# Performance work log

Hardware: AMD Instinct MI355X
Metric: run time of the kernel (lower is better)

## Reference

```python
import jax, jax.numpy as jnp
import numpy as np

H = 512       # hidden_dim == node_init_dim
N_MAX = 128   # max nodes (upper bound on ADD_NODE count)
L = 1024      # action sequence length (padded with -1)
NEG = -1e9    # mask value for invalid destination logits


def _gru(x, h, wih, whh, bih, bhh):
    # PyTorch nn.GRUCell math; gates packed as [r, z, n] along dim 0.
    gi = wih @ x + bih
    gh = whh @ h + bhh
    d = h.shape[0]
    r = jax.nn.sigmoid(gi[:d] + gh[:d])
    z = jax.nn.sigmoid(gi[d:2 * d] + gh[d:2 * d])
    n = jnp.tanh(gi[2 * d:] + r * gh[2 * d:])
    return (1.0 - z) * n + z * h


def _make_actions(rng):
    # Synthesize a grammatically valid DGMG teacher-forcing trace:
    # ADD_NODE=0, ADD_EDGE=1, CHOOSE_DEST=2, STOP_EDGE=3, STOP_NODE=4, pad=-1
    acts, ags = [], []
    cur = -1
    while len(acts) < L - 8 and cur < N_MAX - 1:
        acts.append(0); ags.append(0)
        cur += 1
        if cur > 0:
            for _ in range(int(rng.integers(1, 4))):
                if len(acts) >= L - 4:
                    break
                acts.append(1); ags.append(0)
                acts.append(2); ags.append(int(rng.integers(0, cur)))
            acts.append(3); ags.append(0)
    acts.append(4); ags.append(0)
    pad = L - len(acts)
    acts += [-1] * pad
    ags += [0] * pad
    return np.array(acts, np.int64), np.array(ags, np.int64)


def setup_inputs() -> dict:
    rng = np.random.default_rng(0)
    acts, ags = _make_actions(rng)
    key = jax.random.key(0)
    ks = jax.random.split(key, 12)
    s = 0.02
    p = lambda k, shape: jax.random.normal(k, shape, jnp.float32) * s
    return {
        "actions": jnp.asarray(acts),
        "args_seq": jnp.asarray(ags),
        "node_init": p(ks[0], (H,)),
        "w_nip": p(ks[1], (H, H)), "b_nip": jnp.zeros((H,), jnp.float32),
        "w_e1": p(ks[2], (H, 2 * H)), "b_e1": jnp.zeros((H,), jnp.float32),
        "w_e2": p(ks[3], (2, H)), "b_e2": jnp.zeros((2,), jnp.float32),
        "w_q": p(ks[4], (H, 2 * H)), "b_q": jnp.zeros((H,), jnp.float32),
        "w_k": p(ks[5], (H, H)), "b_k": jnp.zeros((H,), jnp.float32),
        "wih_n": p(ks[6], (3 * H, H)), "whh_n": p(ks[7], (3 * H, H)),
        "bih_n": jnp.zeros((3 * H,), jnp.float32), "bhh_n": jnp.zeros((3 * H,), jnp.float32),
        "wih_g": p(ks[8], (3 * H, H)), "whh_g": p(ks[9], (3 * H, H)),
        "bih_g": jnp.zeros((3 * H,), jnp.float32), "bhh_g": jnp.zeros((3 * H,), jnp.float32),
        "graph0": jnp.zeros((H,), jnp.float32),
    }


def reference(actions, args_seq, node_init, w_nip, b_nip, w_e1, b_e1, w_e2, b_e2,
              w_q, b_q, w_k, b_k, wih_n, whh_n, bih_n, bhh_n,
              wih_g, whh_g, bih_g, bhh_g, graph0):
    h0 = w_nip @ node_init + b_nip  # same fresh-node embedding for every ADD_NODE
    idx_range = jnp.arange(N_MAX)

    def edge_logits(g, curv):
        h = jax.nn.relu(w_e1 @ jnp.concatenate([g, curv]) + b_e1)
        return w_e2 @ h + b_e2  # (2,)

    def add_node(carry, arg):
        g, ne, cur, nll = carry
        cur2 = cur + 1
        ne2 = ne.at[cur2].set(h0)
        g2 = _gru(h0, g, wih_g, whh_g, bih_g, bhh_g)
        return (g2, ne2, cur2, nll)

    def add_edge(carry, arg):
        g, ne, cur, nll = carry
        nll2 = nll - jax.nn.log_softmax(edge_logits(g, ne[cur]))[0]
        return (g, ne, cur, nll2)

    def choose_dest(carry, arg):
        g, ne, cur, nll = carry
        curv = ne[cur]
        q = w_q @ jnp.concatenate([g, curv]) + b_q           # (H,)
        k = ne @ w_k.T + b_k                                  # (N_MAX, H)
        logits = jnp.where(idx_range < cur, k @ q, NEG)       # mask nodes >= cur
        nll2 = nll - jax.nn.log_softmax(logits)[arg]
        chosen = ne[arg]
        new_cur = _gru(chosen, curv, wih_n, whh_n, bih_n, bhh_n)
        ne2 = ne.at[cur].set(new_cur)
        g2 = _gru(new_cur, g, wih_g, whh_g, bih_g, bhh_g)
        return (g2, ne2, cur, nll2)

    def stop_edge(carry, arg):
        g, ne, cur, nll = carry
        nll2 = nll - jax.nn.log_softmax(edge_logits(g, ne[cur]))[1]
        return (g, ne, cur, nll2)

    def noop(carry, arg):
        return carry

    branches = [add_node, add_edge, choose_dest, stop_edge, noop]

    def step(carry, inp):
        a, arg = inp
        idx = jnp.where((a < 0) | (a >= 4), 4, a).astype(jnp.int32)
        return jax.lax.switch(idx, branches, carry, arg), None

    init = (graph0, jnp.zeros((N_MAX, H), graph0.dtype),
            jnp.int32(-1), jnp.zeros((), graph0.dtype))
    (g, ne, cur, nll), _ = jax.lax.scan(
        step, init, (actions.astype(jnp.int32), args_seq.astype(jnp.int32)))
    return nll
```

## Files before the change

kernel.cpp:

```cpp
#include <hip/hip_runtime.h>
#include <math.h>

#define NBLK 64
#define NTHR 704
#define LSEQ 1024

typedef unsigned int u32;
typedef unsigned short u16;
typedef unsigned long long u64;

__device__ __forceinline__ float bf2f(u16 u){ union{u32 i;float f;}v; v.i=(u32)u<<16; return v.f; }
__device__ __forceinline__ u16 f2bf(float f){ union{float f;u32 i;}v; v.f=f; u32 x=v.i;
  return (u16)((x + 0x7fffu + ((x>>16)&1u)) >> 16); }
__device__ __forceinline__ float u2f(u32 u){ union{u32 i;float f;}v; v.i=u; return v.f; }
__device__ __forceinline__ u32  f2u(float f){ union{float f;u32 i;}v; v.f=f; return v.i; }
__device__ __forceinline__ float sigm(float x){ return 1.f/(1.f+__expf(-x)); }

__device__ __forceinline__ u64 gld64(const u64* p){ return __hip_atomic_load(const_cast<u64*>(p), __ATOMIC_RELAXED, __HIP_MEMORY_SCOPE_AGENT); }
__device__ __forceinline__ void gst64(u64* p, u64 v){ __hip_atomic_store(p, v, __ATOMIC_RELAXED, __HIP_MEMORY_SCOPE_AGENT); }
__device__ __forceinline__ u64 pollt(const u64* p, u32 tag){
  u64 v; int n = 0;
  do { v = gld64(p); } while ((u32)(v>>32) != tag && ++n < (1<<20));
  return v;
}

__device__ __forceinline__ float wred(float a){
  a += __int_as_float(__builtin_amdgcn_update_dpp(0, __float_as_int(a), 0x111, 0xf, 0xf, true));
  a += __int_as_float(__builtin_amdgcn_update_dpp(0, __float_as_int(a), 0x112, 0xf, 0xf, true));
  a += __int_as_float(__builtin_amdgcn_update_dpp(0, __float_as_int(a), 0x114, 0xf, 0xf, true));
  a += __int_as_float(__builtin_amdgcn_update_dpp(0, __float_as_int(a), 0x118, 0xf, 0xf, true));
  a += __int_as_float(__builtin_amdgcn_update_dpp(0, __float_as_int(a), 0x142, 0xa, 0xf, true));
  a += __int_as_float(__builtin_amdgcn_update_dpp(0, __float_as_int(a), 0x143, 0xc, 0xf, true));
  return __int_as_float(__builtin_amdgcn_readlane(__float_as_int(a), 63));
}
__device__ __forceinline__ float wredsh(float a){
  #pragma unroll
  for (int off = 32; off; off >>= 1) a += __shfl_xor(a, off);
  return a;
}
__device__ __forceinline__ float wredmaxsh(float a){
  #pragma unroll
  for (int off = 32; off; off >>= 1) a = fmaxf(a, __shfl_xor(a, off));
  return a;
}

__device__ __forceinline__ float dot8p(uint4 w, float4 a, float4 b2){
  float s;
  s  = u2f(w.x<<16)*a.x  + u2f(w.x&0xffff0000u)*a.y;
  s += u2f(w.y<<16)*a.z  + u2f(w.y&0xffff0000u)*a.w;
  s += u2f(w.z<<16)*b2.x + u2f(w.z&0xffff0000u)*b2.y;
  s += u2f(w.w<<16)*b2.z + u2f(w.w&0xffff0000u)*b2.w;
  return s;
}
__device__ __forceinline__ float dot4f(float4 w, float4 x){
  return w.x*x.x + w.y*x.y + w.z*x.z + w.w*x.w;
}
__device__ __forceinline__ uint4 pk8(float4 a, float4 b2){
  uint4 r;
  r.x = (u32)f2bf(a.x)  | ((u32)f2bf(a.y)<<16);
  r.y = (u32)f2bf(a.z)  | ((u32)f2bf(a.w)<<16);
  r.z = (u32)f2bf(b2.x) | ((u32)f2bf(b2.y)<<16);
  r.w = (u32)f2bf(b2.z) | ((u32)f2bf(b2.w)<<16);
  return r;
}

#define SMEM_BYTES 150048

#define RUN_JOBS() do { \
  if (wv == 8 && d2V && (b == d2o1 || b == d2o2)){ \
    int half_ = (b == d2o2) ? 1 : 0; \
    const u64* P_ = XP + ((size_t)(d2Slot*64 + lane))*64 + half_*32; \
    u64 vv_[32]; int bad_; int nn_ = 0; \
    do { bad_ = 0; \
      _Pragma("unroll") for (int j_ = 0; j_ < 32; ++j_) vv_[j_] = gld64(P_ + j_); \
      _Pragma("unroll") for (int j_ = 0; j_ < 32; ++j_) bad_ |= ((u32)(vv_[j_]>>32) != d2Tag); \
    } while (bad_ && ++nn_ < (1<<20)); \
    float h0_ = 0.f, h1_ = 0.f; \
    _Pragma("unroll") for (int j_ = 0; j_ < 32; ++j_){ \
      h0_ += bf2f((u16)(vv_[j_] & 0xffff)); h1_ += bf2f((u16)((vv_[j_]>>16) & 0xffff)); } \
    gst64(&XS[half_*256 + d2Slot*64 + lane], ((u64)d2Tag<<32) | (u32)f2bf(h0_) | ((u32)f2bf(h1_)<<16)); \
  } \
  if (wv == 10 && d3V && b == d3o1){ \
    const u64* pa_ = &XS[d3Slot*64 + lane]; \
    const u64* pb_ = &XS[256 + d3Slot*64 + lane]; \
    u64 va_, vb_; int nn_ = 0; \
    do { va_ = gld64(pa_); vb_ = gld64(pb_); } \
    while ((((u32)(va_>>32) != d3Tag) || ((u32)(vb_>>32) != d3Tag)) && ++nn_ < (1<<20)); \
    float x0 = bf2f((u16)(va_ & 0xffff)) + bf2f((u16)(vb_ & 0xffff)); \
    float x1 = bf2f((u16)((va_>>16) & 0xffff)) + bf2f((u16)((vb_>>16) & 0xffff)); \
    x0 = (lane < d3cur)      ? x0 : -__builtin_inff(); \
    x1 = (lane + 64 < d3cur) ? x1 : -__builtin_inff(); \
    float m_ = wredmaxsh(fmaxf(x0, x1)); \
    float s_ = wredsh(__expf(x0 - m_) + __expf(x1 - m_)); \
    float la_ = (d3arg < 64) ? __shfl(x0, d3arg) : __shfl(x1, d3arg - 64); \
    if (lane == 0) nllw += (m_ + logf(s_)) - la_; \
  } \
  if (wv == 9 && e2V && b == e2Own){ \
    u64 v_ = pollt(XE + e2Slot*64 + lane, e2Tag); \
    float p0_ = wredsh(bf2f((u16)(v_ & 0xffff))); \
    float p1_ = wredsh(bf2f((u16)((v_>>16) & 0xffff))); \
    if (lane == 0){ \
      float l0_ = p0_ + be2_0, l1_ = p1_ + be2_1; \
      float m_ = fmaxf(l0_, l1_); \
      nllw += m_ + logf(__expf(l0_-m_) + __expf(l1_-m_)) - (e2Sel ? l1_ : l0_); \
    } \
  } \
} while(0)

#define SHIFT3() do { \
  d3V=d2V; d3Slot=d2Slot; d3o1=d2o1; d3Tag=d2Tag; d3cur=d2cur; d3arg=d2arg; \
  d2V=d1V; d2Slot=d1Slot; d2o1=d1o1; d2o2=d1o2; d2Tag=d1Tag; d2cur=d1cur; d2arg=d1arg; \
  d1V=0; \
  e2V=e1V; e2Slot=e1Slot; e2Own=e1Own; e2Tag=e1Tag; e2Sel=e1Sel; \
  e1V=0; \
} while(0)

__global__ void __launch_bounds__(NTHR, 1)
dgmg_kernel(const int* __restrict__ actions, const int* __restrict__ argseq,
            const float* __restrict__ node_init, const float* __restrict__ w_nip, const float* __restrict__ b_nip,
            const float* __restrict__ w_e1, const float* __restrict__ b_e1,
            const float* __restrict__ w_e2, const float* __restrict__ b_e2,
            const float* __restrict__ w_q, const float* __restrict__ b_q,
            const float* __restrict__ w_k,
            const float* __restrict__ wih_n, const float* __restrict__ whh_n,
            const float* __restrict__ bih_n, const float* __restrict__ bhh_n,
            const float* __restrict__ wih_g, const float* __restrict__ whh_g,
            const float* __restrict__ bih_g, const float* __restrict__ bhh_g,
            const float* __restrict__ graph0,
            float* __restrict__ out, unsigned char* __restrict__ ws)
{
  extern __shared__ unsigned char smem[];
  u16* s_wihg = (u16*)smem;
  u16* s_whhg = s_wihg + 24*512;
  u16* s_wihn = s_whhg + 24*512;
  u16* s_whhn = s_wihn + 24*512;
  u16* s_we1  = s_whhn + 24*512;
  u16* s_wq   = s_we1 + 8*1024;
  float* s_g    = (float*)(s_wq + 8*1024);
  float* s_nc   = s_g + 512;
  float* s_curv = s_nc + 512;
  float* s_h0   = s_curv + 512;
  float* s_kloc = s_h0 + 512;
  float* s_bihg = s_kloc + 1024;
  float* s_bhhg = s_bihg + 24;
  float* s_bihn = s_bhhg + 24;
  float* s_bhhn = s_bihn + 24;
  float* s_be1  = s_bhhn + 24;
  float* s_bq   = s_be1 + 8;
  float* s_q8   = s_bq + 8;
  float* s_red  = s_q8 + 8;
  u16*   s_gin  = (u16*)(s_red + 16);

  const int b = blockIdx.x, tid = threadIdx.x;
  const int wv = tid >> 6, lane = tid & 63;
  const int d = b*8 + ((wv < 8) ? wv : 0);

  u64* Xng = (u64*)ws;
  u64* Xh  = Xng + 2048;
  u64* XE  = Xh + 512;
  u64* XP  = XE + 256;
  u64* XS  = XP + 16384;
  u64* XN  = XS + 512;

  if (tid < 24){
    int ld = tid/3, gt = tid%3;
    int row = gt*512 + b*8 + ld;
    s_bihg[tid] = bih_g[row]; s_bhhg[tid] = bhh_g[row];
    s_bihn[tid] = bih_n[row]; s_bhhn[tid] = bhh_n[row];
  }
  if (tid < 8){ s_be1[tid] = b_e1[b*8+tid]; s_bq[tid] = b_q[b*8+tid]; }

  for (int r = wv; r < 24; r += 11){
    int ld = r/3, gt = r%3;
    long grow = (long)(gt*512 + b*8 + ld) * 512;
    float4 a0, a1;
    a0 = *(const float4*)&wih_g[grow + lane*8]; a1 = *(const float4*)&wih_g[grow + lane*8 + 4];
    *(uint4*)&s_wihg[r*512 + lane*8] = pk8(a0, a1);
    a0 = *(const float4*)&whh_g[grow + lane*8]; a1 = *(const float4*)&whh_g[grow + lane*8 + 4];
    *(uint4*)&s_whhg[r*512 + lane*8] = pk8(a0, a1);
    a0 = *(const float4*)&wih_n[grow + lane*8]; a1 = *(const float4*)&wih_n[grow + lane*8 + 4];
    *(uint4*)&s_wihn[r*512 + lane*8] = pk8(a0, a1);
    a0 = *(const float4*)&whh_n[grow + lane*8]; a1 = *(const float4*)&whh_n[grow + lane*8 + 4];
    *(uint4*)&s_whhn[r*512 + lane*8] = pk8(a0, a1);
  }
  if (wv < 8){
    long grow = (long)(b*8 + wv) * 1024;
    #pragma unroll
    for (int h = 0; h < 2; ++h){
      float4 a0 = *(const float4*)&w_e1[grow + h*512 + lane*8];
      float4 a1 = *(const float4*)&w_e1[grow + h*512 + lane*8 + 4];
      *(uint4*)&s_we1[wv*1024 + h*512 + lane*8] = pk8(a0, a1);
      float4 q0 = *(const float4*)&w_q[grow + h*512 + lane*8];
      float4 q1 = *(const float4*)&w_q[grow + h*512 + lane*8 + 4];
      *(uint4*)&s_wq[wv*1024 + h*512 + lane*8] = pk8(q0, q1);
    }
  }
  float we2_0 = w_e2[d], we2_1 = w_e2[512+d];
  float be2_0 = b_e2[0], be2_1 = b_e2[1];
  float nllw = 0.f;

  int d1V=0,d1Slot=0,d1o1=0,d1o2=0,d1cur=0,d1arg=0; u32 d1Tag=0;
  int d2V=0,d2Slot=0,d2o1=0,d2o2=0,d2cur=0,d2arg=0; u32 d2Tag=0;
  int d3V=0,d3Slot=0,d3o1=0,d3cur=0,d3arg=0; u32 d3Tag=0;
  int e1V=0,e1Slot=0,e1Own=0,e1Sel=0; u32 e1Tag=0;
  int e2V=0,e2Slot=0,e2Own=0,e2Sel=0; u32 e2Tag=0;
  int ecnt=0, dcnt=0;

  if (tid < 512) s_g[tid] = node_init[tid];
  __syncthreads();
  float cbg_r=0,cbg_z=0,bg_ni=0,bg_nh=0, bh_gr=0,bh_gz=0;
  float bn_r=0,bn_z=0,bn_nh=0, fb_r=0,fb_z=0,fb_n=0, be1w=0,bqw=0;
  if (wv < 8){
    cbg_r = s_bihg[wv*3+0]+s_bhhg[wv*3+0];
    cbg_z = s_bihg[wv*3+1]+s_bhhg[wv*3+1];
    bg_ni = s_bihg[wv*3+2]; bg_nh = s_bhhg[wv*3+2];
    bh_gr = s_bhhg[wv*3+0]; bh_gz = s_bhhg[wv*3+1];
    bn_r = s_bhhn[wv*3+0]; bn_z = s_bhhn[wv*3+1]; bn_nh = s_bhhn[wv*3+2];
    fb_r = s_bihn[wv*3+0]; fb_z = s_bihn[wv*3+1]; fb_n = s_bihn[wv*3+2];
    be1w = s_be1[wv]; bqw = s_bq[wv];
    const float* wr = w_nip + (long)d*512;
    float4 wa = *(const float4*)&wr[lane*8], wb2 = *(const float4*)&wr[lane*8+4];
    float4 xa = *(float4*)&s_g[lane*8], xb = *(float4*)&s_g[lane*8+4];
    float h0d = wred(dot4f(wa,xa)+dot4f(wb2,xb)) + b_nip[d];
    if (lane == 0) gst64(&Xh[d], (1ull<<32) | f2u(h0d));
  }
  __syncthreads();
  u32 ph = 2;

  float gi0r=0,gi0z=0,gi0n=0, ghn0r=0,ghn0z=0,ghn0n=0;
  int cur = -1, have_se = 0;
  bool first_an = true;

  for (int t = 0; t < LSEQ; ++t){
    int a = actions[t];
    if (a == 1) continue;
    if (a == 3){ have_se = 1; continue; }
    if (a < 0 || a >= 4) continue;

    int t1 = (t+1 < LSEQ) ? actions[t+1] : -1;
    int nxt = (t1 == 1);
    int i2 = (t+2 < LSEQ) ? t+2 : LSEQ-1;
    int chn = nxt ? argseq[i2] : 0;

    u32 tg = ph-1;

    if (a == 0){
      int eslot = ecnt & 3;
      if (first_an){
        if (tid < 512){ u64 v = pollt(&Xh[tid], 1u); s_h0[tid] = u2f((u32)v); s_g[tid] = graph0[tid]; }
      } else {
        if (tid < 512){ u64 v = pollt(&Xng[((tg&1)*512+tid)*2+1], tg); s_g[tid] = u2f((u32)v); }
      }
      __syncthreads();
      RUN_JOBS();
      if (wv < 8){
        float4 xg_a = *(float4*)&s_g[lane*8], xg_b = *(float4*)&s_g[lane*8+4];
        float4 xc_a = *(float4*)&s_curv[lane*8], xc_b = *(float4*)&s_curv[lane*8+4];
        const u32* Whg = (const u32*)s_whhg;
        if (first_an){
          float4 xh_a = *(float4*)&s_h0[lane*8], xh_b = *(float4*)&s_h0[lane*8+4];
          const u32* Wig = (const u32*)s_wihg; const u32* Wn = (const u32*)s_whhn;
          gi0r = wred(dot8p(*(const uint4*)&Wig[(wv*3+0)*256+lane*4], xh_a,xh_b)) + s_bihg[wv*3+0];
          gi0z = wred(dot8p(*(const uint4*)&Wig[(wv*3+1)*256+lane*4], xh_a,xh_b)) + s_bihg[wv*3+1];
          gi0n = wred(dot8p(*(const uint4*)&Wig[(wv*3+2)*256+lane*4], xh_a,xh_b)) + s_bihg[wv*3+2];
          ghn0r = wred(dot8p(*(const uint4*)&Wn[(wv*3+0)*256+lane*4], xh_a,xh_b)) + bn_r;
          ghn0z = wred(dot8p(*(const uint4*)&Wn[(wv*3+1)*256+lane*4], xh_a,xh_b)) + bn_z;
          ghn0n = wred(dot8p(*(const uint4*)&Wn[(wv*3+2)*256+lane*4], xh_a,xh_b)) + bn_nh;
        }
        {
          float ghr = wred(dot8p(*(const uint4*)&Whg[(wv*3+0)*256+lane*4], xg_a,xg_b)) + bh_gr;
          float ghz = wred(dot8p(*(const uint4*)&Whg[(wv*3+1)*256+lane*4], xg_a,xg_b)) + bh_gz;
          float ghn = wred(dot8p(*(const uint4*)&Whg[(wv*3+2)*256+lane*4], xg_a,xg_b)) + bg_nh;
          float r_ = sigm(gi0r + ghr), z_ = sigm(gi0z + ghz);
          float n_ = tanhf(gi0n + r_*ghn);
          if (lane == 0) gst64(&Xng[((ph&1)*512+d)*2+1], ((u64)ph<<32) | f2u((1.f-z_)*n_ + z_*s_g[d]));
        }
        float fr=0.f, fz=0.f, fn=0.f;
        if (cur >= 0){
          const u32* Win = (const u32*)s_wihn;
          fr = wred(dot8p(*(const uint4*)&Win[(wv*3+0)*256+lane*4], xc_a,xc_b)) + fb_r;
          fz = wred(dot8p(*(const uint4*)&Win[(wv*3+1)*256+lane*4], xc_a,xc_b)) + fb_z;
          fn = wred(dot8p(*(const uint4*)&Win[(wv*3+2)*256+lane*4], xc_a,xc_b)) + fb_n;
          const float* wkr = w_k + (long)d*512;
          float4 ka = *(const float4*)&wkr[lane*8], kb2 = *(const float4*)&wkr[lane*8+4];
          float kv = wred(dot4f(ka,xc_a)+dot4f(kb2,xc_b));
          if (lane == 0){
            s_gin[cur*24+wv*3+0] = f2bf(fr); s_gin[cur*24+wv*3+1] = f2bf(fz); s_gin[cur*24+wv*3+2] = f2bf(fn);
            s_kloc[wv*128 + cur] = kv;
          }
        }
        if (nxt){
          float gr = (chn == cur) ? fr : bf2f(s_gin[chn*24+wv*3+0]);
          float gz = (chn == cur) ? fz : bf2f(s_gin[chn*24+wv*3+1]);
          float gn = (chn == cur) ? fn : bf2f(s_gin[chn*24+wv*3+2]);
          float r2 = sigm(gr + ghn0r), z2 = sigm(gz + ghn0z);
          float n2 = tanhf(gn + r2*ghn0n);
          if (lane == 0) gst64(&Xng[((ph&1)*512+d)*2], ((u64)ph<<32) | f2u((1.f-z2)*n2 + z2*s_h0[d]));
        }
        if (have_se){
          const u32* Re = (const u32*)s_we1 + wv*512;
          float pe = dot8p(*(const uint4*)&Re[lane*4], xg_a,xg_b) + dot8p(*(const uint4*)&Re[256+lane*4], xc_a,xc_b);
          float hv = fmaxf(wred(pe) + be1w, 0.f);
          if (lane == 0){ s_red[wv*2] = hv*we2_0; s_red[wv*2+1] = hv*we2_1; }
        }
      }
      __syncthreads();
      if (have_se && tid == 0){
        float p0 = 0.f, p1 = 0.f;
        #pragma unroll
        for (int i = 0; i < 8; ++i){ p0 += s_red[i*2]; p1 += s_red[i*2+1]; }
        gst64(&XE[eslot*64 + b], ((u64)ph<<32) | (u32)f2bf(p0) | ((u32)f2bf(p1)<<16));
      }
      if (tid < 512) s_curv[tid] = s_h0[tid];
      SHIFT3();
      if (have_se){ e1V=1; e1Slot=eslot; e1Sel=1; e1Own=ecnt&63; e1Tag=ph; ecnt++; }
      have_se = 0; first_an = false;
      cur += 1; ph += 1;
    }
    else {
      int arg = argseq[t];
      int eslot = ecnt & 3, dslot = dcnt & 3;
      if (tid < 512){
        const u64* p = &Xng[((tg&1)*512 + tid)*2];
        u64 v0, v1; int n = 0;
        do { v0 = gld64(p); v1 = gld64(p+1); }
        while ((((u32)(v0>>32) != tg) || ((u32)(v1>>32) != tg)) && ++n < (1<<20));
        s_nc[tid] = u2f((u32)v0); s_g[tid] = u2f((u32)v1);
      }
      __syncthreads();
      RUN_JOBS();
      if (wv < 8){
        float4 xn_a = *(float4*)&s_nc[lane*8], xn_b = *(float4*)&s_nc[lane*8+4];
        float4 xg_a = *(float4*)&s_g[lane*8],  xg_b = *(float4*)&s_g[lane*8+4];
        float4 xc_a = *(float4*)&s_curv[lane*8], xc_b = *(float4*)&s_curv[lane*8+4];
        const u32* Wn = (const u32*)s_whhn; const u32* Wig = (const u32*)s_wihg; const u32* Whg = (const u32*)s_whhg;
        {
          float pr = dot8p(*(const uint4*)&Wig[(wv*3+0)*256+lane*4], xn_a,xn_b)
                   + dot8p(*(const uint4*)&Whg[(wv*3+0)*256+lane*4], xg_a,xg_b);
          float pz = dot8p(*(const uint4*)&Wig[(wv*3+1)*256+lane*4], xn_a,xn_b)
                   + dot8p(*(const uint4*)&Whg[(wv*3+1)*256+lane*4], xg_a,xg_b);
          float r_ = sigm(wred(pr) + cbg_r);
          float z_ = sigm(wred(pz) + cbg_z);
          float gin_ = wred(dot8p(*(const uint4*)&Wig[(wv*3+2)*256+lane*4], xn_a,xn_b)) + bg_ni;
          float ghn_ = wred(dot8p(*(const uint4*)&Whg[(wv*3+2)*256+lane*4], xg_a,xg_b)) + bg_nh;
          float n_ = tanhf(gin_ + r_*ghn_);
          if (lane == 0) gst64(&Xng[((ph&1)*512+d)*2+1], ((u64)ph<<32) | f2u((1.f-z_)*n_ + z_*s_g[d]));
        }
        if (nxt){
          float ghr = wred(dot8p(*(const uint4*)&Wn[(wv*3+0)*256+lane*4], xn_a,xn_b)) + bn_r;
          float ghz = wred(dot8p(*(const uint4*)&Wn[(wv*3+1)*256+lane*4], xn_a,xn_b)) + bn_z;
          float ghn = wred(dot8p(*(const uint4*)&Wn[(wv*3+2)*256+lane*4], xn_a,xn_b)) + bn_nh;
          float gr = bf2f(s_gin[chn*24+wv*3+0]), gz = bf2f(s_gin[chn*24+wv*3+1]), gn = bf2f(s_gin[chn*24+wv*3+2]);
          float r_ = sigm(gr+ghr), z_ = sigm(gz+ghz);
          float n_ = tanhf(gn + r_*ghn);
          if (lane == 0) gst64(&Xng[((ph&1)*512+d)*2], ((u64)ph<<32) | f2u((1.f-z_)*n_ + z_*s_nc[d]));
        }
        {
          const u32* Rq = (const u32*)s_wq + wv*512;
          float pq = dot8p(*(const uint4*)&Rq[lane*4], xg_a,xg_b) + dot8p(*(const uint4*)&Rq[256+lane*4], xc_a,xc_b);
          float qd = wred(pq) + bqw;
          const u32* Re = (const u32*)s_we1 + wv*512;
          float pe = dot8p(*(const uint4*)&Re[lane*4], xg_a,xg_b) + dot8p(*(const uint4*)&Re[256+lane*4], xc_a,xc_b);
          float hv = fmaxf(wred(pe) + be1w, 0.f);
          if (lane == 0){ s_q8[wv] = qd; s_red[wv*2] = hv*we2_0; s_red[wv*2+1] = hv*we2_1; }
        }
      }
      __syncthreads();
      if (tid < 64){
        float pl0 = 0.f, pl1 = 0.f;
        #pragma unroll
        for (int k = 0; k < 8; ++k){
          pl0 += s_kloc[k*128 + tid]      * s_q8[k];
          pl1 += s_kloc[k*128 + tid + 64] * s_q8[k];
        }
        gst64(&XP[((size_t)(dslot*64 + tid))*64 + b], ((u64)ph<<32) | (u32)f2bf(pl0) | ((u32)f2bf(pl1)<<16));
      }
      if (tid == 64){
        float p0 = 0.f, p1 = 0.f;
        #pragma unroll
        for (int i = 0; i < 8; ++i){ p0 += s_red[i*2]; p1 += s_red[i*2+1]; }
        gst64(&XE[eslot*64 + b], ((u64)ph<<32) | (u32)f2bf(p0) | ((u32)f2bf(p1)<<16));
      }
      if (tid < 512) s_curv[tid] = s_nc[tid];
      SHIFT3();
      e1V=1; e1Slot=eslot; e1Sel=0; e1Own=ecnt&63; e1Tag=ph; ecnt++;
      d1V=1; d1Slot=dslot; d1o1=(2*dcnt)&63; d1o2=(2*dcnt+1)&63; d1cur=cur; d1arg=arg; d1Tag=ph; dcnt++;
      ph += 1;
    }
  }

  {
    int eslot = ecnt & 3;
    u32 tg = ph-1;
    if (tid < 512){ u64 v = pollt(&Xng[((tg&1)*512+tid)*2+1], tg); s_g[tid] = u2f((u32)v); }
    __syncthreads();
    RUN_JOBS();
    if (have_se && wv < 8){
      float4 xg_a = *(float4*)&s_g[lane*8], xg_b = *(float4*)&s_g[lane*8+4];
      float4 xc_a = *(float4*)&s_curv[lane*8], xc_b = *(float4*)&s_curv[lane*8+4];
      const u32* Re = (const u32*)s_we1 + wv*512;
      float pe = dot8p(*(const uint4*)&Re[lane*4], xg_a,xg_b) + dot8p(*(const uint4*)&Re[256+lane*4], xc_a,xc_b);
      float hv = fmaxf(wred(pe) + be1w, 0.f);
      if (lane == 0){ s_red[wv*2] = hv*we2_0; s_red[wv*2+1] = hv*we2_1; }
    }
    __syncthreads();
    if (have_se && tid == 0){
      float p0 = 0.f, p1 = 0.f;
      #pragma unroll
      for (int i = 0; i < 8; ++i){ p0 += s_red[i*2]; p1 += s_red[i*2+1]; }
      gst64(&XE[eslot*64 + b], ((u64)ph<<32) | (u32)f2bf(p0) | ((u32)f2bf(p1)<<16));
    }
    SHIFT3();
    if (have_se){ e1V=1; e1Slot=eslot; e1Sel=1; e1Own=ecnt&63; e1Tag=ph; ecnt++; }
    ph += 1;
  }
  #pragma unroll 1
  for (int dp = 0; dp < 3; ++dp){
    __syncthreads();
    RUN_JOBS();
    SHIFT3();
    ph += 1;
  }
  if (wv == 9  && lane == 0) gst64(&XN[b],      (0xFFFFull<<32) | f2u(nllw));
  if (wv == 10 && lane == 0) gst64(&XN[64 + b], (0xFFFFull<<32) | f2u(nllw));
  if (b == 0 && wv == 8){
    u64 va = pollt(&XN[lane], 0xFFFFu);
    u64 vb = pollt(&XN[64 + lane], 0xFFFFu);
    float tot = wredsh(u2f((u32)va) + u2f((u32)vb));
    if (lane == 0) out[0] = tot;
  }
}

extern "C" void kernel_launch(void* const* d_in, const int* in_sizes, int n_in,
                              void* d_out, int out_size, void* d_ws, size_t ws_size,
                              hipStream_t stream) {
  (void)in_sizes; (void)n_in; (void)out_size; (void)ws_size;
  hipMemsetAsync(d_ws, 0, 158720, stream);
  hipFuncSetAttribute((const void*)dgmg_kernel,
                      hipFuncAttributeMaxDynamicSharedMemorySize, SMEM_BYTES);
  dgmg_kernel<<<NBLK, NTHR, SMEM_BYTES, stream>>>(
      (const int*)d_in[0], (const int*)d_in[1],
      (const float*)d_in[2], (const float*)d_in[3], (const float*)d_in[4],
      (const float*)d_in[5], (const float*)d_in[6],
      (const float*)d_in[7], (const float*)d_in[8],
      (const float*)d_in[9], (const float*)d_in[10],
      (const float*)d_in[11],
      (const float*)d_in[13], (const float*)d_in[14],
      (const float*)d_in[15], (const float*)d_in[16],
      (const float*)d_in[17], (const float*)d_in[18],
      (const float*)d_in[19], (const float*)d_in[20],
      (const float*)d_in[21],
      (float*)d_out, (unsigned char*)d_ws);
}
```

Baseline: 1.220 ms.

## Replace per-step block barriers with LDS flag handoff between specialized waves

Removes the __syncthreads barriers in each sequence step. Compute waves now poll the global state directly into registers instead of staging it through shared memory. Waves 8 and 9 are signalled through workgroup-scope acquire/release flags in LDS, and the reduction buffers become multi-buffered by phase so compute waves can run ahead of the helper waves. The former wave-10 job is folded into wave 9, which drops one wave per block, and the ring buffers are deepened. The intent is to cut barrier latency on the serial critical path, at the cost of more spin-polling and tighter ordering requirements that could cause races.

```diff
diff --git a/kernel.cpp b/kernel.cpp
--- a/kernel.cpp
+++ b/kernel.cpp
@@ -2,7 +2,7 @@
 #include <math.h>
 
 #define NBLK 64
-#define NTHR 704
+#define NTHR 640
 #define LSEQ 1024
 
 typedef unsigned int u32;
@@ -22,6 +22,11 @@
   u64 v; int n = 0;
   do { v = gld64(p); } while ((u32)(v>>32) != tag && ++n < (1<<20));
   return v;
+}
+__device__ __forceinline__ u32 lldw(const u32* p){ return __hip_atomic_load(const_cast<u32*>(p), __ATOMIC_ACQUIRE, __HIP_MEMORY_SCOPE_WORKGROUP); }
+__device__ __forceinline__ void lstw(u32* p, u32 v){ __hip_atomic_store(p, v, __ATOMIC_RELEASE, __HIP_MEMORY_SCOPE_WORKGROUP); }
+__device__ __forceinline__ void lwait(const u32* p, int target){
+  int n=0; while ((int)lldw(p) < target){ if(++n > (1<<20)) break; }
 }
 
 __device__ __forceinline__ float wred(float a){
@@ -63,24 +68,50 @@
   r.w = (u32)f2bf(b2.z) | ((u32)f2bf(b2.w)<<16);
   return r;
 }
-
-#define SMEM_BYTES 150048
-
-#define RUN_JOBS() do { \
-  if (wv == 8 && d2V && (b == d2o1 || b == d2o2)){ \
+__device__ __forceinline__ float sel8(float4 a, float4 b2, int i){
+  float lo = (i&2) ? ((i&1)? a.w : a.z) : ((i&1)? a.y : a.x);
+  float hi = (i&2) ? ((i&1)? b2.w : b2.z) : ((i&1)? b2.y : b2.x);
+  return (i&4) ? hi : lo;
+}
+
+#define SMEM_BYTES 142208
+
+#define SHIFT() do { \
+  d3V=d2V; d3Slot=d2Slot; d3o1=d2o1; d3Tag=d2Tag; d3cur=d2cur; d3arg=d2arg; \
+  d2V=d1V; d2Slot=d1Slot; d2o1=d1o1; d2o2=d1o2; d2Tag=d1Tag; d2cur=d1cur; d2arg=d1arg; \
+  d1V=0; \
+  e2V=e1V; e2Slot=e1Slot; e2Own=e1Own; e2Tag=e1Tag; e2Sel=e1Sel; \
+  e1V=0; \
+} while(0)
+
+#define W8_DA() do { \
+  if (d2V && (b == d2o1 || b == d2o2)){ \
     int half_ = (b == d2o2) ? 1 : 0; \
     const u64* P_ = XP + ((size_t)(d2Slot*64 + lane))*64 + half_*32; \
     u64 vv_[32]; int bad_; int nn_ = 0; \
     do { bad_ = 0; \
       _Pragma("unroll") for (int j_ = 0; j_ < 32; ++j_) vv_[j_] = gld64(P_ + j_); \
-      _Pragma("unroll") for (int j_ = 0; j_ < 32; ++j_) bad_ |= ((u32)(vv_[j_]>>32) != d2Tag); \
+      _Pragma("unroll") for (int j_ = 0; j_ < 32; ++j_) bad_ |= (int)((u32)(vv_[j_]>>32) != d2Tag); \
     } while (bad_ && ++nn_ < (1<<20)); \
     float h0_ = 0.f, h1_ = 0.f; \
     _Pragma("unroll") for (int j_ = 0; j_ < 32; ++j_){ \
       h0_ += bf2f((u16)(vv_[j_] & 0xffff)); h1_ += bf2f((u16)((vv_[j_]>>16) & 0xffff)); } \
     gst64(&XS[half_*256 + d2Slot*64 + lane], ((u64)d2Tag<<32) | (u32)f2bf(h0_) | ((u32)f2bf(h1_)<<16)); \
   } \
-  if (wv == 10 && d3V && b == d3o1){ \
+} while(0)
+
+#define W9_JOBS() do { \
+  if (e2V && b == e2Own){ \
+    u64 v_ = pollt(XE + e2Slot*64 + lane, e2Tag); \
+    float p0_ = wredsh(bf2f((u16)(v_ & 0xffff))); \
+    float p1_ = wredsh(bf2f((u16)((v_>>16) & 0xffff))); \
+    if (lane == 0){ \
+      float l0_ = p0_ + be2_0, l1_ = p1_ + be2_1; \
+      float m_ = fmaxf(l0_, l1_); \
+      nllw += m_ + logf(__expf(l0_-m_) + __expf(l1_-m_)) - (e2Sel ? l1_ : l0_); \
+    } \
+  } \
+  if (d3V && b == d3o1){ \
     const u64* pa_ = &XS[d3Slot*64 + lane]; \
     const u64* pb_ = &XS[256 + d3Slot*64 + lane]; \
     u64 va_, vb_; int nn_ = 0; \
@@ -95,24 +126,6 @@
     float la_ = (d3arg < 64) ? __shfl(x0, d3arg) : __shfl(x1, d3arg - 64); \
     if (lane == 0) nllw += (m_ + logf(s_)) - la_; \
   } \
-  if (wv == 9 && e2V && b == e2Own){ \
-    u64 v_ = pollt(XE + e2Slot*64 + lane, e2Tag); \
-    float p0_ = wredsh(bf2f((u16)(v_ & 0xffff))); \
-    float p1_ = wredsh(bf2f((u16)((v_>>16) & 0xffff))); \
-    if (lane == 0){ \
-      float l0_ = p0_ + be2_0, l1_ = p1_ + be2_1; \
-      float m_ = fmaxf(l0_, l1_); \
-      nllw += m_ + logf(__expf(l0_-m_) + __expf(l1_-m_)) - (e2Sel ? l1_ : l0_); \
-    } \
-  } \
-} while(0)
-
-#define SHIFT3() do { \
-  d3V=d2V; d3Slot=d2Slot; d3o1=d2o1; d3Tag=d2Tag; d3cur=d2cur; d3arg=d2arg; \
-  d2V=d1V; d2Slot=d1Slot; d2o1=d1o1; d2o2=d1o2; d2Tag=d1Tag; d2cur=d1cur; d2arg=d1arg; \
-  d1V=0; \
-  e2V=e1V; e2Slot=e1Slot; e2Own=e1Own; e2Tag=e1Tag; e2Sel=e1Sel; \
-  e1V=0; \
 } while(0)
 
 __global__ void __launch_bounds__(NTHR, 1)
@@ -136,29 +149,28 @@
   u16* s_whhn = s_wihn + 24*512;
   u16* s_we1  = s_whhn + 24*512;
   u16* s_wq   = s_we1 + 8*1024;
-  float* s_g    = (float*)(s_wq + 8*1024);
-  float* s_nc   = s_g + 512;
-  float* s_curv = s_nc + 512;
-  float* s_h0   = s_curv + 512;
-  float* s_kloc = s_h0 + 512;
-  float* s_bihg = s_kloc + 1024;
+  float* s_kloc = (float*)(s_wq + 8*1024);
+  u16*   s_gin  = (u16*)(s_kloc + 1024);
+  float* s_bihg = (float*)(s_gin + 128*24);
   float* s_bhhg = s_bihg + 24;
   float* s_bihn = s_bhhg + 24;
   float* s_bhhn = s_bihn + 24;
   float* s_be1  = s_bhhn + 24;
   float* s_bq   = s_be1 + 8;
   float* s_q8   = s_bq + 8;
-  float* s_red  = s_q8 + 8;
-  u16*   s_gin  = (u16*)(s_red + 16);
+  float* s_red  = s_q8 + 32;
+  u32*   s_wfl  = (u32*)(s_red + 64);
+  u32*   s_w8d  = s_wfl + 8;
+  u32*   s_w9d  = s_w8d + 1;
 
   const int b = blockIdx.x, tid = threadIdx.x;
   const int wv = tid >> 6, lane = tid & 63;
   const int d = b*8 + ((wv < 8) ? wv : 0);
 
   u64* Xng = (u64*)ws;
-  u64* Xh  = Xng + 2048;
+  u64* Xh  = Xng + 4096;
   u64* XE  = Xh + 512;
-  u64* XP  = XE + 256;
+  u64* XP  = XE + 512;
   u64* XS  = XP + 16384;
   u64* XN  = XS + 512;
 
@@ -169,8 +181,13 @@
     s_bihn[tid] = bih_n[row]; s_bhhn[tid] = bhh_n[row];
   }
   if (tid < 8){ s_be1[tid] = b_e1[b*8+tid]; s_bq[tid] = b_q[b*8+tid]; }
-
-  for (int r = wv; r < 24; r += 11){
+  if (tid == 0){
+    #pragma unroll
+    for (int w = 0; w < 8; ++w) s_wfl[w] = 1u;
+    s_w8d[0] = 1u; s_w9d[0] = 1u;
+  }
+
+  for (int r = wv; r < 24; r += 10){
     int ld = r/3, gt = r%3;
     long grow = (long)(gt*512 + b*8 + ld) * 512;
     float4 a0, a1;
@@ -195,19 +212,12 @@
       *(uint4*)&s_wq[wv*1024 + h*512 + lane*8] = pk8(q0, q1);
     }
   }
+  __syncthreads();
+
   float we2_0 = w_e2[d], we2_1 = w_e2[512+d];
   float be2_0 = b_e2[0], be2_1 = b_e2[1];
   float nllw = 0.f;
 
-  int d1V=0,d1Slot=0,d1o1=0,d1o2=0,d1cur=0,d1arg=0; u32 d1Tag=0;
-  int d2V=0,d2Slot=0,d2o1=0,d2o2=0,d2cur=0,d2arg=0; u32 d2Tag=0;
-  int d3V=0,d3Slot=0,d3o1=0,d3cur=0,d3arg=0; u32 d3Tag=0;
-  int e1V=0,e1Slot=0,e1Own=0,e1Sel=0; u32 e1Tag=0;
-  int e2V=0,e2Slot=0,e2Own=0,e2Sel=0; u32 e2Tag=0;
-  int ecnt=0, dcnt=0;
-
-  if (tid < 512) s_g[tid] = node_init[tid];
-  __syncthreads();
   float cbg_r=0,cbg_z=0,bg_ni=0,bg_nh=0, bh_gr=0,bh_gz=0;
   float bn_r=0,bn_z=0,bn_nh=0, fb_r=0,fb_z=0,fb_n=0, be1w=0,bqw=0;
   if (wv < 8){
@@ -218,16 +228,26 @@
     bn_r = s_bhhn[wv*3+0]; bn_z = s_bhhn[wv*3+1]; bn_nh = s_bhhn[wv*3+2];
     fb_r = s_bihn[wv*3+0]; fb_z = s_bihn[wv*3+1]; fb_n = s_bihn[wv*3+2];
     be1w = s_be1[wv]; bqw = s_bq[wv];
+    float4 xa = *(const float4*)&node_init[lane*8];
+    float4 xb = *(const float4*)&node_init[lane*8+4];
     const float* wr = w_nip + (long)d*512;
     float4 wa = *(const float4*)&wr[lane*8], wb2 = *(const float4*)&wr[lane*8+4];
-    float4 xa = *(float4*)&s_g[lane*8], xb = *(float4*)&s_g[lane*8+4];
     float h0d = wred(dot4f(wa,xa)+dot4f(wb2,xb)) + b_nip[d];
     if (lane == 0) gst64(&Xh[d], (1ull<<32) | f2u(h0d));
   }
-  __syncthreads();
   u32 ph = 2;
 
+  float4 h0_a = make_float4(0,0,0,0), h0_b = make_float4(0,0,0,0);
+  float4 xc_a = make_float4(0,0,0,0), xc_b = make_float4(0,0,0,0);
   float gi0r=0,gi0z=0,gi0n=0, ghn0r=0,ghn0z=0,ghn0n=0;
+
+  int d1V=0,d1Slot=0,d1o1=0,d1o2=0,d1cur=0,d1arg=0; u32 d1Tag=0;
+  int d2V=0,d2Slot=0,d2o1=0,d2o2=0,d2cur=0,d2arg=0; u32 d2Tag=0;
+  int d3V=0,d3Slot=0,d3o1=0,d3cur=0,d3arg=0; u32 d3Tag=0;
+  int e1V=0,e1Slot=0,e1Own=0,e1Sel=0; u32 e1Tag=0;
+  int e2V=0,e2Slot=0,e2Own=0,e2Sel=0; u32 e2Tag=0;
+  int ecnt=0, dcnt=0;
+
   int cur = -1, have_se = 0;
   bool first_an = true;
 
@@ -242,42 +262,17 @@
     int i2 = (t+2 < LSEQ) ? t+2 : LSEQ-1;
     int chn = nxt ? argseq[i2] : 0;
 
-    u32 tg = ph-1;
+    u32 tg = ph-1; int ps = (int)(tg&3), pf = (int)(ph&3);
+    { int n=0; while ((int)lldw(s_w8d) < (int)ph-1){ if(++n>(1<<20)) break; } }
+    { int n=0; while ((int)lldw(s_w9d) < (int)ph-2){ if(++n>(1<<20)) break; } }
 
     if (a == 0){
-      int eslot = ecnt & 3;
-      if (first_an){
-        if (tid < 512){ u64 v = pollt(&Xh[tid], 1u); s_h0[tid] = u2f((u32)v); s_g[tid] = graph0[tid]; }
-      } else {
-        if (tid < 512){ u64 v = pollt(&Xng[((tg&1)*512+tid)*2+1], tg); s_g[tid] = u2f((u32)v); }
-      }
-      __syncthreads();
-      RUN_JOBS();
+      int se = have_se;
+      int eslot = ecnt & 7;
       if (wv < 8){
-        float4 xg_a = *(float4*)&s_g[lane*8], xg_b = *(float4*)&s_g[lane*8+4];
-        float4 xc_a = *(float4*)&s_curv[lane*8], xc_b = *(float4*)&s_curv[lane*8+4];
-        const u32* Whg = (const u32*)s_whhg;
-        if (first_an){
-          float4 xh_a = *(float4*)&s_h0[lane*8], xh_b = *(float4*)&s_h0[lane*8+4];
-          const u32* Wig = (const u32*)s_wihg; const u32* Wn = (const u32*)s_whhn;
-          gi0r = wred(dot8p(*(const uint4*)&Wig[(wv*3+0)*256+lane*4], xh_a,xh_b)) + s_bihg[wv*3+0];
-          gi0z = wred(dot8p(*(const uint4*)&Wig[(wv*3+1)*256+lane*4], xh_a,xh_b)) + s_bihg[wv*3+1];
-          gi0n = wred(dot8p(*(const uint4*)&Wig[(wv*3+2)*256+lane*4], xh_a,xh_b)) + s_bihg[wv*3+2];
-          ghn0r = wred(dot8p(*(const uint4*)&Wn[(wv*3+0)*256+lane*4], xh_a,xh_b)) + bn_r;
-          ghn0z = wred(dot8p(*(const uint4*)&Wn[(wv*3+1)*256+lane*4], xh_a,xh_b)) + bn_z;
-          ghn0n = wred(dot8p(*(const uint4*)&Wn[(wv*3+2)*256+lane*4], xh_a,xh_b)) + bn_nh;
-        }
-        {
-          float ghr = wred(dot8p(*(const uint4*)&Whg[(wv*3+0)*256+lane*4], xg_a,xg_b)) + bh_gr;
-          float ghz = wred(dot8p(*(const uint4*)&Whg[(wv*3+1)*256+lane*4], xg_a,xg_b)) + bh_gz;
-          float ghn = wred(dot8p(*(const uint4*)&Whg[(wv*3+2)*256+lane*4], xg_a,xg_b)) + bg_nh;
-          float r_ = sigm(gi0r + ghr), z_ = sigm(gi0z + ghz);
-          float n_ = tanhf(gi0n + r_*ghn);
-          if (lane == 0) gst64(&Xng[((ph&1)*512+d)*2+1], ((u64)ph<<32) | f2u((1.f-z_)*n_ + z_*s_g[d]));
-        }
+        const u32* Win = (const u32*)s_wihn;
         float fr=0.f, fz=0.f, fn=0.f;
         if (cur >= 0){
-          const u32* Win = (const u32*)s_wihn;
           fr = wred(dot8p(*(const uint4*)&Win[(wv*3+0)*256+lane*4], xc_a,xc_b)) + fb_r;
           fz = wred(dot8p(*(const uint4*)&Win[(wv*3+1)*256+lane*4], xc_a,xc_b)) + fb_z;
           fn = wred(dot8p(*(const uint4*)&Win[(wv*3+2)*256+lane*4], xc_a,xc_b)) + fb_n;
@@ -290,49 +285,112 @@
           }
         }
         if (nxt){
-          float gr = (chn == cur) ? fr : bf2f(s_gin[chn*24+wv*3+0]);
-          float gz = (chn == cur) ? fz : bf2f(s_gin[chn*24+wv*3+1]);
-          float gn = (chn == cur) ? fn : bf2f(s_gin[chn*24+wv*3+2]);
+          float gr = (chn == cur && cur >= 0) ? fr : bf2f(s_gin[chn*24+wv*3+0]);
+          float gz = (chn == cur && cur >= 0) ? fz : bf2f(s_gin[chn*24+wv*3+1]);
+          float gn = (chn == cur && cur >= 0) ? fn : bf2f(s_gin[chn*24+wv*3+2]);
           float r2 = sigm(gr + ghn0r), z2 = sigm(gz + ghn0z);
           float n2 = tanhf(gn + r2*ghn0n);
-          if (lane == 0) gst64(&Xng[((ph&1)*512+d)*2], ((u64)ph<<32) | f2u((1.f-z2)*n2 + z2*s_h0[d]));
-        }
-        if (have_se){
+          float h0d = __shfl(sel8(h0_a, h0_b, wv), b);
+          if (lane == 0) gst64(&Xng[((size_t)pf*512+d)*2], ((u64)ph<<32) | f2u((1.f-z2)*n2 + z2*h0d));
+        }
+        float4 xg_a, xg_b;
+        if (first_an){
+          u64 v[8]; int nn=0;
+          const u64* P = Xh + lane*8;
+          for (;;){
+            #pragma unroll
+            for (int k = 0; k < 8; ++k) v[k] = gld64(P + k);
+            int ok = 1;
+            #pragma unroll
+            for (int k = 0; k < 8; ++k) ok &= (int)((u32)(v[k]>>32) == 1u);
+            if (__all(ok)) break;
+            if (++nn > (1<<20)) break;
+          }
+          h0_a = make_float4(u2f((u32)v[0]),u2f((u32)v[1]),u2f((u32)v[2]),u2f((u32)v[3]));
+          h0_b = make_float4(u2f((u32)v[4]),u2f((u32)v[5]),u2f((u32)v[6]),u2f((u32)v[7]));
+          xg_a = *(const float4*)&graph0[lane*8];
+          xg_b = *(const float4*)&graph0[lane*8+4];
+          const u32* Wig = (const u32*)s_wihg; const u32* Wn = (const u32*)s_whhn;
+          gi0r = wred(dot8p(*(const uint4*)&Wig[(wv*3+0)*256+lane*4], h0_a,h0_b)) + s_bihg[wv*3+0];
+          gi0z = wred(dot8p(*(const uint4*)&Wig[(wv*3+1)*256+lane*4], h0_a,h0_b)) + s_bihg[wv*3+1];
+          gi0n = wred(dot8p(*(const uint4*)&Wig[(wv*3+2)*256+lane*4], h0_a,h0_b)) + s_bihg[wv*3+2];
+          ghn0r = wred(dot8p(*(const uint4*)&Wn[(wv*3+0)*256+lane*4], h0_a,h0_b)) + bn_r;
+          ghn0z = wred(dot8p(*(const uint4*)&Wn[(wv*3+1)*256+lane*4], h0_a,h0_b)) + bn_z;
+          ghn0n = wred(dot8p(*(const uint4*)&Wn[(wv*3+2)*256+lane*4], h0_a,h0_b)) + bn_nh;
+        } else {
+          u64 v[8]; int nn=0;
+          const u64* P = Xng + ((size_t)ps*512 + lane*8)*2 + 1;
+          for (;;){
+            #pragma unroll
+            for (int k = 0; k < 8; ++k) v[k] = gld64(P + 2*k);
+            int ok = 1;
+            #pragma unroll
+            for (int k = 0; k < 8; ++k) ok &= (int)((u32)(v[k]>>32) == tg);
+            if (__all(ok)) break;
+            if (++nn > (1<<20)) break;
+          }
+          xg_a = make_float4(u2f((u32)v[0]),u2f((u32)v[1]),u2f((u32)v[2]),u2f((u32)v[3]));
+          xg_b = make_float4(u2f((u32)v[4]),u2f((u32)v[5]),u2f((u32)v[6]),u2f((u32)v[7]));
+        }
+        {
+          const u32* Whg = (const u32*)s_whhg;
+          float ghr = wred(dot8p(*(const uint4*)&Whg[(wv*3+0)*256+lane*4], xg_a,xg_b)) + bh_gr;
+          float ghz = wred(dot8p(*(const uint4*)&Whg[(wv*3+1)*256+lane*4], xg_a,xg_b)) + bh_gz;
+          float ghn = wred(dot8p(*(const uint4*)&Whg[(wv*3+2)*256+lane*4], xg_a,xg_b)) + bg_nh;
+          float r_ = sigm(gi0r + ghr), z_ = sigm(gi0z + ghz);
+          float n_ = tanhf(gi0n + r_*ghn);
+          float gd = __shfl(sel8(xg_a, xg_b, wv), b);
+          if (lane == 0) gst64(&Xng[((size_t)pf*512+d)*2+1], ((u64)ph<<32) | f2u((1.f-z_)*n_ + z_*gd));
+        }
+        if (se){
           const u32* Re = (const u32*)s_we1 + wv*512;
           float pe = dot8p(*(const uint4*)&Re[lane*4], xg_a,xg_b) + dot8p(*(const uint4*)&Re[256+lane*4], xc_a,xc_b);
           float hv = fmaxf(wred(pe) + be1w, 0.f);
-          if (lane == 0){ s_red[wv*2] = hv*we2_0; s_red[wv*2+1] = hv*we2_1; }
-        }
-      }
-      __syncthreads();
-      if (have_se && tid == 0){
-        float p0 = 0.f, p1 = 0.f;
-        #pragma unroll
-        for (int i = 0; i < 8; ++i){ p0 += s_red[i*2]; p1 += s_red[i*2+1]; }
-        gst64(&XE[eslot*64 + b], ((u64)ph<<32) | (u32)f2bf(p0) | ((u32)f2bf(p1)<<16));
-      }
-      if (tid < 512) s_curv[tid] = s_h0[tid];
-      SHIFT3();
-      if (have_se){ e1V=1; e1Slot=eslot; e1Sel=1; e1Own=ecnt&63; e1Tag=ph; ecnt++; }
+          if (lane == 0){ s_red[pf*16 + wv*2] = hv*we2_0; s_red[pf*16 + wv*2+1] = hv*we2_1; }
+        }
+        xc_a = h0_a; xc_b = h0_b;
+        if (lane == 0) lstw(&s_wfl[wv], ph);
+      }
+      if (wv == 8){
+        W8_DA();
+        #pragma unroll 1
+        for (int w = 0; w < 8; ++w) lwait(&s_wfl[w], (int)ph);
+        if (se && lane == 0){
+          float p0 = 0.f, p1 = 0.f;
+          #pragma unroll
+          for (int i = 0; i < 8; ++i){ p0 += s_red[pf*16 + i*2]; p1 += s_red[pf*16 + i*2+1]; }
+          gst64(&XE[eslot*64 + b], ((u64)ph<<32) | (u32)f2bf(p0) | ((u32)f2bf(p1)<<16));
+        }
+        if (lane == 0) lstw(s_w8d, ph);
+      }
+      if (wv == 9){
+        W9_JOBS();
+        if (lane == 0) lstw(s_w9d, ph);
+      }
+      SHIFT();
+      if (se){ e1V=1; e1Slot=eslot; e1Sel=1; e1Own=ecnt&63; e1Tag=ph; ecnt++; }
       have_se = 0; first_an = false;
       cur += 1; ph += 1;
     }
     else {
       int arg = argseq[t];
-      int eslot = ecnt & 3, dslot = dcnt & 3;
-      if (tid < 512){
-        const u64* p = &Xng[((tg&1)*512 + tid)*2];
-        u64 v0, v1; int n = 0;
-        do { v0 = gld64(p); v1 = gld64(p+1); }
-        while ((((u32)(v0>>32) != tg) || ((u32)(v1>>32) != tg)) && ++n < (1<<20));
-        s_nc[tid] = u2f((u32)v0); s_g[tid] = u2f((u32)v1);
-      }
-      __syncthreads();
-      RUN_JOBS();
+      int eslot = ecnt & 7, dslot = dcnt & 3;
       if (wv < 8){
-        float4 xn_a = *(float4*)&s_nc[lane*8], xn_b = *(float4*)&s_nc[lane*8+4];
-        float4 xg_a = *(float4*)&s_g[lane*8],  xg_b = *(float4*)&s_g[lane*8+4];
-        float4 xc_a = *(float4*)&s_curv[lane*8], xc_b = *(float4*)&s_curv[lane*8+4];
+        u64 v[16]; int nn=0;
+        const u64* P = Xng + ((size_t)ps*512 + lane*8)*2;
+        for (;;){
+          #pragma unroll
+          for (int k = 0; k < 16; ++k) v[k] = gld64(P + k);
+          int ok = 1;
+          #pragma unroll
+          for (int k = 0; k < 16; ++k) ok &= (int)((u32)(v[k]>>32) == tg);
+          if (__all(ok)) break;
+          if (++nn > (1<<20)) break;
+        }
+        float4 xn_a = make_float4(u2f((u32)v[0]), u2f((u32)v[2]), u2f((u32)v[4]), u2f((u32)v[6]));
+        float4 xn_b = make_float4(u2f((u32)v[8]), u2f((u32)v[10]),u2f((u32)v[12]),u2f((u32)v[14]));
+        float4 xg_a = make_float4(u2f((u32)v[1]), u2f((u32)v[3]), u2f((u32)v[5]), u2f((u32)v[7]));
+        float4 xg_b = make_float4(u2f((u32)v[9]), u2f((u32)v[11]),u2f((u32)v[13]),u2f((u32)v[15]));
         const u32* Wn = (const u32*)s_whhn; const u32* Wig = (const u32*)s_wihg; const u32* Whg = (const u32*)s_whhg;
         {
           float pr = dot8p(*(const uint4*)&Wig[(wv*3+0)*256+lane*4], xn_a,xn_b)
@@ -344,7 +402,8 @@
           float gin_ = wred(dot8p(*(const uint4*)&Wig[(wv*3+2)*256+lane*4], xn_a,xn_b)) + bg_ni;
           float ghn_ = wred(dot8p(*(const uint4*)&Whg[(wv*3+2)*256+lane*4], xg_a,xg_b)) + bg_nh;
           float n_ = tanhf(gin_ + r_*ghn_);
-          if (lane == 0) gst64(&Xng[((ph&1)*512+d)*2+1], ((u64)ph<<32) | f2u((1.f-z_)*n_ + z_*s_g[d]));
+          float gd = __shfl(sel8(xg_a, xg_b, wv), b);
+          if (lane == 0) gst64(&Xng[((size_t)pf*512+d)*2+1], ((u64)ph<<32) | f2u((1.f-z_)*n_ + z_*gd));
         }
         if (nxt){
           float ghr = wred(dot8p(*(const uint4*)&Wn[(wv*3+0)*256+lane*4], xn_a,xn_b)) + bn_r;
@@ -353,7 +412,8 @@
           float gr = bf2f(s_gin[chn*24+wv*3+0]), gz = bf2f(s_gin[chn*24+wv*3+1]), gn = bf2f(s_gin[chn*24+wv*3+2]);
           float r_ = sigm(gr+ghr), z_ = sigm(gz+ghz);
           float n_ = tanhf(gn + r_*ghn);
-          if (lane == 0) gst64(&Xng[((ph&1)*512+d)*2], ((u64)ph<<32) | f2u((1.f-z_)*n_ + z_*s_nc[d]));
+          float ncd = __shfl(sel8(xn_a, xn_b, wv), b);
+          if (lane == 0) gst64(&Xng[((size_t)pf*512+d)*2], ((u64)ph<<32) | f2u((1.f-z_)*n_ + z_*ncd));
         }
         {
           const u32* Rq = (const u32*)s_wq + wv*512;
@@ -362,27 +422,38 @@
           const u32* Re = (const u32*)s_we1 + wv*512;
           float pe = dot8p(*(const uint4*)&Re[lane*4], xg_a,xg_b) + dot8p(*(const uint4*)&Re[256+lane*4], xc_a,xc_b);
           float hv = fmaxf(wred(pe) + be1w, 0.f);
-          if (lane == 0){ s_q8[wv] = qd; s_red[wv*2] = hv*we2_0; s_red[wv*2+1] = hv*we2_1; }
-        }
-      }
-      __syncthreads();
-      if (tid < 64){
-        float pl0 = 0.f, pl1 = 0.f;
-        #pragma unroll
-        for (int k = 0; k < 8; ++k){
-          pl0 += s_kloc[k*128 + tid]      * s_q8[k];
-          pl1 += s_kloc[k*128 + tid + 64] * s_q8[k];
-        }
-        gst64(&XP[((size_t)(dslot*64 + tid))*64 + b], ((u64)ph<<32) | (u32)f2bf(pl0) | ((u32)f2bf(pl1)<<16));
-      }
-      if (tid == 64){
-        float p0 = 0.f, p1 = 0.f;
-        #pragma unroll
-        for (int i = 0; i < 8; ++i){ p0 += s_red[i*2]; p1 += s_red[i*2+1]; }
-        gst64(&XE[eslot*64 + b], ((u64)ph<<32) | (u32)f2bf(p0) | ((u32)f2bf(p1)<<16));
-      }
-      if (tid < 512) s_curv[tid] = s_nc[tid];
-      SHIFT3();
+          if (lane == 0){ s_q8[pf*8+wv] = qd; s_red[pf*16+wv*2] = hv*we2_0; s_red[pf*16+wv*2+1] = hv*we2_1; }
+        }
+        xc_a = xn_a; xc_b = xn_b;
+        if (lane == 0) lstw(&s_wfl[wv], ph);
+      }
+      if (wv == 8){
+        W8_DA();
+        #pragma unroll 1
+        for (int w = 0; w < 8; ++w) lwait(&s_wfl[w], (int)ph);
+        {
+          float pl0 = 0.f, pl1 = 0.f;
+          #pragma unroll
+          for (int k = 0; k < 8; ++k){
+            float qk = s_q8[pf*8 + k];
+            pl0 += s_kloc[k*128 + lane]      * qk;
+            pl1 += s_kloc[k*128 + lane + 64] * qk;
+          }
+          gst64(&XP[((size_t)(dslot*64 + lane))*64 + b], ((u64)ph<<32) | (u32)f2bf(pl0) | ((u32)f2bf(pl1)<<16));
+        }
+        if (lane == 0){
+          float p0 = 0.f, p1 = 0.f;
+          #pragma unroll
+          for (int i = 0; i < 8; ++i){ p0 += s_red[pf*16 + i*2]; p1 += s_red[pf*16 + i*2+1]; }
+          gst64(&XE[eslot*64 + b], ((u64)ph<<32) | (u32)f2bf(p0) | ((u32)f2bf(p1)<<16));
+        }
+        if (lane == 0) lstw(s_w8d, ph);
+      }
+      if (wv == 9){
+        W9_JOBS();
+        if (lane == 0) lstw(s_w9d, ph);
+      }
+      SHIFT();
       e1V=1; e1Slot=eslot; e1Sel=0; e1Own=ecnt&63; e1Tag=ph; ecnt++;
       d1V=1; d1Slot=dslot; d1o1=(2*dcnt)&63; d1o2=(2*dcnt+1)&63; d1cur=cur; d1arg=arg; d1Tag=ph; dcnt++;
       ph += 1;
@@ -390,44 +461,80 @@
   }
 
   {
-    int eslot = ecnt & 3;
-    u32 tg = ph-1;
-    if (tid < 512){ u64 v = pollt(&Xng[((tg&1)*512+tid)*2+1], tg); s_g[tid] = u2f((u32)v); }
-    __syncthreads();
-    RUN_JOBS();
-    if (have_se && wv < 8){
-      float4 xg_a = *(float4*)&s_g[lane*8], xg_b = *(float4*)&s_g[lane*8+4];
-      float4 xc_a = *(float4*)&s_curv[lane*8], xc_b = *(float4*)&s_curv[lane*8+4];
-      const u32* Re = (const u32*)s_we1 + wv*512;
-      float pe = dot8p(*(const uint4*)&Re[lane*4], xg_a,xg_b) + dot8p(*(const uint4*)&Re[256+lane*4], xc_a,xc_b);
-      float hv = fmaxf(wred(pe) + be1w, 0.f);
-      if (lane == 0){ s_red[wv*2] = hv*we2_0; s_red[wv*2+1] = hv*we2_1; }
-    }
-    __syncthreads();
-    if (have_se && tid == 0){
-      float p0 = 0.f, p1 = 0.f;
-      #pragma unroll
-      for (int i = 0; i < 8; ++i){ p0 += s_red[i*2]; p1 += s_red[i*2+1]; }
-      gst64(&XE[eslot*64 + b], ((u64)ph<<32) | (u32)f2bf(p0) | ((u32)f2bf(p1)<<16));
-    }
-    SHIFT3();
-    if (have_se){ e1V=1; e1Slot=eslot; e1Sel=1; e1Own=ecnt&63; e1Tag=ph; ecnt++; }
+    int se = have_se;
+    int eslot = ecnt & 7;
+    u32 tg = ph-1; int ps = (int)(tg&3), pf = (int)(ph&3);
+    { int n=0; while ((int)lldw(s_w8d) < (int)ph-1){ if(++n>(1<<20)) break; } }
+    { int n=0; while ((int)lldw(s_w9d) < (int)ph-2){ if(++n>(1<<20)) break; } }
+    if (wv < 8){
+      u64 v[8]; int nn=0;
+      const u64* P = Xng + ((size_t)ps*512 + lane*8)*2 + 1;
+      for (;;){
+        #pragma unroll
+        for (int k = 0; k < 8; ++k) v[k] = gld64(P + 2*k);
+        int ok = 1;
+        #pragma unroll
+        for (int k = 0; k < 8; ++k) ok &= (int)((u32)(v[k]>>32) == tg);
+        if (__all(ok)) break;
+        if (++nn > (1<<20)) break;
+      }
+      if (se){
+        float4 xg_a = make_float4(u2f((u32)v[0]),u2f((u32)v[1]),u2f((u32)v[2]),u2f((u32)v[3]));
+        float4 xg_b = make_float4(u2f((u32)v[4]),u2f((u32)v[5]),u2f((u32)v[6]),u2f((u32)v[7]));
+        const u32* Re = (const u32*)s_we1 + wv*512;
+        float pe = dot8p(*(const uint4*)&Re[lane*4], xg_a,xg_b) + dot8p(*(const uint4*)&Re[256+lane*4], xc_a,xc_b);
+        float hv = fmaxf(wred(pe) + be1w, 0.f);
+        if (lane == 0){ s_red[pf*16+wv*2] = hv*we2_0; s_red[pf*16+wv*2+1] = hv*we2_1; }
+      }
+      if (lane == 0) lstw(&s_wfl[wv], ph);
+    }
+    if (wv == 8){
+      W8_DA();
+      #pragma unroll 1
+      for (int w = 0; w < 8; ++w) lwait(&s_wfl[w], (int)ph);
+      if (se && lane == 0){
+        float p0 = 0.f, p1 = 0.f;
+        #pragma unroll
+        for (int i = 0; i < 8; ++i){ p0 += s_red[pf*16 + i*2]; p1 += s_red[pf*16 + i*2+1]; }
+        gst64(&XE[eslot*64 + b], ((u64)ph<<32) | (u32)f2bf(p0) | ((u32)f2bf(p1)<<16));
+      }
+      if (lane == 0) lstw(s_w8d, ph);
+    }
+    if (wv == 9){
+      W9_JOBS();
+      if (lane == 0) lstw(s_w9d, ph);
+    }
+    SHIFT();
+    if (se){ e1V=1; e1Slot=eslot; e1Sel=1; e1Own=ecnt&63; e1Tag=ph; ecnt++; }
     ph += 1;
   }
   #pragma unroll 1
-  for (int dp = 0; dp < 3; ++dp){
-    __syncthreads();
-    RUN_JOBS();
-    SHIFT3();
+  for (int dp = 0; dp < 4; ++dp){
+    { int n=0; while ((int)lldw(s_w8d) < (int)ph-1){ if(++n>(1<<20)) break; } }
+    { int n=0; while ((int)lldw(s_w9d) < (int)ph-2){ if(++n>(1<<20)) break; } }
+    if (wv < 8){
+      if (lane == 0) lstw(&s_wfl[wv], ph);
+    }
+    if (wv == 8){
+      W8_DA();
+      #pragma unroll 1
+      for (int w = 0; w < 8; ++w) lwait(&s_wfl[w], (int)ph);
+      if (lane == 0) lstw(s_w8d, ph);
+    }
+    if (wv == 9){
+      W9_JOBS();
+      if (lane == 0) lstw(s_w9d, ph);
+    }
+    SHIFT();
     ph += 1;
   }
-  if (wv == 9  && lane == 0) gst64(&XN[b],      (0xFFFFull<<32) | f2u(nllw));
-  if (wv == 10 && lane == 0) gst64(&XN[64 + b], (0xFFFFull<<32) | f2u(nllw));
-  if (b == 0 && wv == 8){
-    u64 va = pollt(&XN[lane], 0xFFFFu);
-    u64 vb = pollt(&XN[64 + lane], 0xFFFFu);
-    float tot = wredsh(u2f((u32)va) + u2f((u32)vb));
-    if (lane == 0) out[0] = tot;
+  if (wv == 9){
+    if (lane == 0) gst64(&XN[b], (0xFFFFull<<32) | f2u(nllw));
+    if (b == 0){
+      u64 v = pollt(&XN[lane], 0xFFFFu);
+      float tot = wredsh(u2f((u32)v));
+      if (lane == 0) out[0] = tot;
+    }
   }
 }
 
@@ -435,7 +542,7 @@
                               void* d_out, int out_size, void* d_ws, size_t ws_size,
                               hipStream_t stream) {
   (void)in_sizes; (void)n_in; (void)out_size; (void)ws_size;
-  hipMemsetAsync(d_ws, 0, 158720, stream);
+  hipMemsetAsync(d_ws, 0, 176640, stream);
   hipFuncSetAttribute((const void*)dgmg_kernel,
                       hipFuncAttributeMaxDynamicSharedMemorySize, SMEM_BYTES);
   dgmg_kernel<<<NBLK, NTHR, SMEM_BYTES, stream>>>(
```

New measurement: 2.637 ms. 2.16x slower.
